# Kernel optimization log

Measured on AMD Instinct MI355X. Metric: run time of the kernel, lower is better.

## Reference

```python
import jax, jax.numpy as jnp
import numpy as np
from functools import partial

B, C, H, W = 16, 512, 38, 50
IMG_H, IMG_W = 608, 800
STRIDE = 16
IMG_SCALE = 1.0
MIN_SIZE = 16.0 * IMG_SCALE
PRE_NMS_TOP_N = 6000
POST_NMS_TOP_N = 300
NMS_THRESH = 0.7


def generate_anchor_base(base_size=16.0, ratios=(0.5, 1.0, 2.0), scales=(8.0, 16.0, 32.0)):
    # chainercv-style base anchors centered at (base/2, base/2), y1x1y2x2
    py = px = base_size / 2.0
    out = []
    for r in ratios:
        for s in scales:
            h = base_size * s * np.sqrt(r)
            w = base_size * s * np.sqrt(1.0 / r)
            out.append([py - h / 2, px - w / 2, py + h / 2, px + w / 2])
    return jnp.asarray(np.array(out, dtype=np.float32))  # [9, 4]


def all_anchors(anchor_base, stride, h, w):
    sy = jnp.arange(h, dtype=jnp.float32) * stride
    sx = jnp.arange(w, dtype=jnp.float32) * stride
    yy, xx = jnp.meshgrid(sy, sx, indexing='ij')
    shifts = jnp.stack([yy, xx, yy, xx], axis=-1).reshape(-1, 1, 4)  # [H*W,1,4]
    return (shifts + anchor_base[None]).reshape(-1, 4)  # [H*W*9, 4]


def conv2d(x, w, b, pad):
    y = jax.lax.conv_general_dilated(
        x, w, window_strides=(1, 1), padding=[(pad, pad), (pad, pad)],
        dimension_numbers=('NCHW', 'OIHW', 'NCHW'))
    return y + b[None, :, None, None]


def decode_boxes(anchors, loc):
    # anchors [N,4] y1x1y2x2, loc [B,N,4] (dy,dx,dh,dw)
    ah = anchors[:, 2] - anchors[:, 0]
    aw = anchors[:, 3] - anchors[:, 1]
    acy = anchors[:, 0] + 0.5 * ah
    acx = anchors[:, 1] + 0.5 * aw
    cy = loc[..., 0] * ah + acy
    cx = loc[..., 1] * aw + acx
    h = jnp.exp(loc[..., 2]) * ah
    w = jnp.exp(loc[..., 3]) * aw
    return jnp.stack([cy - 0.5 * h, cx - 0.5 * w, cy + 0.5 * h, cx + 0.5 * w], axis=-1)


def nms_fixed(boxes, scores, iou_thresh, max_out):
    # boxes [N,4], scores [N] (-inf = invalid); greedy NMS, fixed max_out steps
    areas = jnp.clip(boxes[:, 2] - boxes[:, 0], 0) * jnp.clip(boxes[:, 3] - boxes[:, 1], 0)

    def step(valid, _):
        s = jnp.where(valid, scores, -jnp.inf)
        i = jnp.argmax(s)
        ok = jnp.isfinite(s[i])
        box = boxes[i]
        yy1 = jnp.maximum(box[0], boxes[:, 0])
        xx1 = jnp.maximum(box[1], boxes[:, 1])
        yy2 = jnp.minimum(box[2], boxes[:, 2])
        xx2 = jnp.minimum(box[3], boxes[:, 3])
        inter = jnp.clip(yy2 - yy1, 0) * jnp.clip(xx2 - xx1, 0)
        iou = inter / (areas + areas[i] - inter + 1e-9)
        valid = valid & (iou <= iou_thresh)
        valid = valid.at[i].set(False)
        return valid, (i, ok)

    valid0 = jnp.isfinite(scores)
    _, (idx, ok) = jax.lax.scan(step, valid0, None, length=max_out)
    return idx, ok


def proposal_single(boxes, scores):
    # boxes [N,4], scores [N] for one image
    # clip to image
    boxes = jnp.stack([
        jnp.clip(boxes[:, 0], 0.0, IMG_H), jnp.clip(boxes[:, 1], 0.0, IMG_W),
        jnp.clip(boxes[:, 2], 0.0, IMG_H), jnp.clip(boxes[:, 3], 0.0, IMG_W)], axis=-1)
    hs = boxes[:, 2] - boxes[:, 0]
    ws = boxes[:, 3] - boxes[:, 1]
    keep = (hs >= MIN_SIZE) & (ws >= MIN_SIZE)
    scores = jnp.where(keep, scores, -jnp.inf)
    top_s, top_i = jax.lax.top_k(scores, PRE_NMS_TOP_N)
    top_b = boxes[top_i]
    idx, ok = nms_fixed(top_b, top_s, NMS_THRESH, POST_NMS_TOP_N)
    okf = ok.astype(boxes.dtype)
    rois = top_b[idx] * okf[:, None]
    rsc = jnp.where(ok, top_s[idx], 0.0)
    return jnp.concatenate([rois, rsc[:, None]], axis=-1)  # [POST, 5]


def setup_inputs() -> dict:
    key = jax.random.key(0)
    ks = jax.random.split(key, 7)
    return {
        'x': jax.random.normal(ks[0], (B, C, H, W), jnp.float32),
        'share_w': jax.random.normal(ks[1], (512, 512, 3, 3), jnp.float32) * 0.02,
        'share_b': jnp.zeros((512,), jnp.float32),
        'cls_w': jax.random.normal(ks[2], (18, 512, 1, 1), jnp.float32) * 0.02,
        'cls_b': jnp.zeros((18,), jnp.float32),
        'reg_w': jax.random.normal(ks[3], (36, 512, 1, 1), jnp.float32) * 0.02,
        'reg_b': jnp.zeros((36,), jnp.float32),
    }


def reference(x, share_w, share_b, cls_w, cls_b, reg_w, reg_b):
    anchors = all_anchors(generate_anchor_base(), STRIDE, H, W)  # [H*W*9, 4]
    shared = jax.nn.relu(conv2d(x, share_w, share_b, 1))
    cls = conv2d(shared, cls_w, cls_b, 0)           # [B,18,H,W]
    # note: original _reshape is a no-op (view result discarded), so softmax is over all 18 channels
    cls = jax.nn.softmax(cls, axis=1)
    reg = conv2d(shared, reg_w, reg_b, 0)           # [B,36,H,W]
    # foreground scores: [B,18,H,W] -> [B,H,W,9,2] -> fg channel
    scores = cls.transpose(0, 2, 3, 1).reshape(B, H * W * 9, 2)[..., 1]
    loc = reg.transpose(0, 2, 3, 1).reshape(B, H * W * 9, 4)
    boxes = decode_boxes(anchors, loc)              # [B,N,4]
    rois = jax.vmap(proposal_single)(boxes, scores)  # [B,POST,5]
    return rois
```

## Files before the change

kernel.cpp:

```cpp
#include <hip/hip_runtime.h>
#include <math.h>

#define NB 16
#define NC 512
#define NH 38
#define NW 50
#define NHW 1900
#define NPOS 30400
#define NANCH 17100
#define PRE_N 6000
#define POST_N 300
#define KTOT 4608
#define IMGH 608.0f
#define IMGW 800.0f

__global__ __launch_bounds__(256)
void conv_f64_v3(const float* __restrict__ x, const float* __restrict__ w,
                 const float* __restrict__ bias, float* __restrict__ out)
{
    const int b    = blockIdx.z;
    const int co0  = blockIdx.y * 128;
    const int pos0 = blockIdx.x * 64;

    __shared__ __align__(16) double Ad[8][130];
    __shared__ __align__(16) double Bd[8][66];

    const int tid = threadIdx.x;
    const int ty  = tid >> 4;
    const int tx  = tid & 15;

    double acc[8][4];
#pragma unroll
    for (int m = 0; m < 8; ++m)
#pragma unroll
        for (int n = 0; n < 4; ++n) acc[m][n] = 0.0;

    const float* xb = x + (size_t)b * NC * NHW;

    const int coiA = tid >> 1;
    const int k4A  = (tid & 1) * 4;
    const int kk2B = (tid >> 6) * 2;
    const int piB  = tid & 63;
    const int slotB = ((piB & 3) << 4) + (piB >> 2);
    const int pB   = pos0 + piB;
    const int pyB  = pB / NW;
    const int pxB  = pB - pyB * NW;

    for (int k0 = 0; k0 < KTOT; k0 += 8) {
        const float4 wa = *reinterpret_cast<const float4*>(
            &w[(size_t)(co0 + coiA) * KTOT + k0 + k4A]);
        float bs[2];
#pragma unroll
        for (int j = 0; j < 2; ++j) {
            const int k  = k0 + kk2B + j;
            const int ci = k / 9;
            const int rr = k - ci * 9;
            const int ky = rr / 3;
            const int kx = rr - ky * 3;
            const int yy = pyB + ky - 1;
            const int xx = pxB + kx - 1;
            float v = 0.f;
            if (pB < NHW && (unsigned)yy < (unsigned)NH && (unsigned)xx < (unsigned)NW)
                v = xb[(size_t)ci * NHW + yy * NW + xx];
            bs[j] = v;
        }
        __syncthreads();
        Ad[k4A + 0][coiA] = (double)wa.x;
        Ad[k4A + 1][coiA] = (double)wa.y;
        Ad[k4A + 2][coiA] = (double)wa.z;
        Ad[k4A + 3][coiA] = (double)wa.w;
        Bd[kk2B + 0][slotB] = (double)bs[0];
        Bd[kk2B + 1][slotB] = (double)bs[1];
        __syncthreads();

#pragma unroll
        for (int kk = 0; kk < 8; ++kk) {
            double av[8], bv[4];
#pragma unroll
            for (int m = 0; m < 8; ++m) av[m] = Ad[kk][ty * 8 + m];
#pragma unroll
            for (int n = 0; n < 4; ++n) bv[n] = Bd[kk][n * 16 + tx];
#pragma unroll
            for (int m = 0; m < 8; ++m)
#pragma unroll
                for (int n = 0; n < 4; ++n) acc[m][n] += av[m] * bv[n];
        }
        __syncthreads();
    }

    const int pos = pos0 + tx * 4;
#pragma unroll
    for (int m = 0; m < 8; ++m) {
        const int co = co0 + ty * 8 + m;
        const double bi = (double)bias[co];
        if (pos < NHW) {
            float* orow = out + ((size_t)b * NC + co) * NHW;
            float4 v;
            double d0 = acc[m][0] + bi;
            double d1 = acc[m][1] + bi;
            double d2 = acc[m][2] + bi;
            double d3 = acc[m][3] + bi;
            v.x = (float)(d0 > 0.0 ? d0 : 0.0);
            v.y = (float)(d1 > 0.0 ? d1 : 0.0);
            v.z = (float)(d2 > 0.0 ? d2 : 0.0);
            v.w = (float)(d3 > 0.0 ? d3 : 0.0);
            *reinterpret_cast<float4*>(&orow[pos]) = v;
        }
    }
}

__global__ __launch_bounds__(256)
void head_f64(const float* __restrict__ act,
              const float* __restrict__ cls_w, const float* __restrict__ cls_b,
              const float* __restrict__ reg_w, const float* __restrict__ reg_b,
              float* __restrict__ boxes, float* __restrict__ scores)
{
    const int p = blockIdx.x * 256 + threadIdx.x;
    if (p >= NPOS) return;
    const int b  = p / NHW;
    const int hw = p - b * NHW;

    const float* av = act + (size_t)b * NC * NHW + hw;

    double acc[54];
#pragma unroll
    for (int o = 0; o < 54; ++o) acc[o] = 0.0;

    for (int c = 0; c < NC; ++c) {
        const double v = (double)av[(size_t)c * NHW];
#pragma unroll
        for (int o = 0; o < 18; ++o) acc[o]      += v * (double)cls_w[o * NC + c];
#pragma unroll
        for (int o = 0; o < 36; ++o) acc[18 + o] += v * (double)reg_w[o * NC + c];
    }

    float lg[18];
#pragma unroll
    for (int o = 0; o < 18; ++o) lg[o] = (float)(acc[o] + (double)cls_b[o]);
    float loc[36];
#pragma unroll
    for (int o = 0; o < 36; ++o) loc[o] = (float)(acc[18 + o] + (double)reg_b[o]);

    double mx = -1e300;
#pragma unroll
    for (int o = 0; o < 18; ++o) mx = fmax(mx, (double)lg[o]);
    double sum = 0.0;
#pragma unroll
    for (int o = 0; o < 18; ++o) sum += exp((double)lg[o] - mx);
    const double inv = 1.0 / sum;

    const int hy = hw / NW;
    const int hx = hw - hy * NW;
    const float shy = (float)(hy * 16);
    const float shx = (float)(hx * 16);

    const double rats[3] = {0.5, 1.0, 2.0};
    const double scls[3] = {8.0, 16.0, 32.0};

#pragma unroll
    for (int a = 0; a < 9; ++a) {
        const int ir = a / 3, is = a - ir * 3;
        const double hh = 16.0 * scls[is] * sqrt(rats[ir]);
        const double wd = 16.0 * scls[is] * sqrt(1.0 / rats[ir]);
        const float ay1 = (float)(8.0 - hh * 0.5) + shy;
        const float ax1 = (float)(8.0 - wd * 0.5) + shx;
        const float ay2 = (float)(8.0 + hh * 0.5) + shy;
        const float ax2 = (float)(8.0 + wd * 0.5) + shx;
        const float ahf = ay2 - ay1;
        const float awf = ax2 - ax1;
        const float acy = ay1 + 0.5f * ahf;
        const float acx = ax1 + 0.5f * awf;

        const double ah = (double)ahf, aw = (double)awf;
        const double dy = (double)loc[4 * a + 0];
        const double dx = (double)loc[4 * a + 1];
        const double dh = (double)loc[4 * a + 2];
        const double dw = (double)loc[4 * a + 3];
        const double cy = dy * ah + (double)acy;
        const double cx = dx * aw + (double)acx;
        const double bh = exp(dh) * ah;
        const double bw = exp(dw) * aw;
        float y1 = (float)(cy - 0.5 * bh);
        float x1 = (float)(cx - 0.5 * bw);
        float y2 = (float)(cy + 0.5 * bh);
        float x2 = (float)(cx + 0.5 * bw);
        y1 = fminf(fmaxf(y1, 0.f), IMGH);
        y2 = fminf(fmaxf(y2, 0.f), IMGH);
        x1 = fminf(fmaxf(x1, 0.f), IMGW);
        x2 = fminf(fmaxf(x2, 0.f), IMGW);
        const bool keep = ((y2 - y1) >= 16.0f) && ((x2 - x1) >= 16.0f);

        float sc = (float)(exp((double)lg[2 * a + 1] - mx) * inv);
        if (!keep) sc = -INFINITY;

        const int n = hw * 9 + a;
        float4 bx; bx.x = y1; bx.y = x1; bx.z = y2; bx.w = x2;
        *reinterpret_cast<float4*>(&boxes[((size_t)b * NANCH + n) * 4]) = bx;
        scores[(size_t)b * NANCH + n] = sc;
    }
}

__global__ __launch_bounds__(256)
void rank2(const float* __restrict__ scores, const float* __restrict__ boxes,
           float* __restrict__ sortedS, float* __restrict__ sortedB)
{
    const int b = blockIdx.y;
    const int i = blockIdx.x * 256 + threadIdx.x;
    if (i >= NANCH) return;
    const float si = scores[(size_t)b * NANCH + i];
    const float* sb = scores + (size_t)b * NANCH;
    int rank = 0;
    for (int j = 0; j < NANCH; ++j) {
        const float sj = sb[j];
        rank += (sj > si) || (sj == si && j < i);
    }
    if (rank < PRE_N) {
        sortedS[(size_t)b * PRE_N + rank] = si;
        const float4 bx = *reinterpret_cast<const float4*>(&boxes[((size_t)b * NANCH + i) * 4]);
        *reinterpret_cast<float4*>(&sortedB[((size_t)b * PRE_N + rank) * 4]) = bx;
    }
}

__global__ __launch_bounds__(64)
void nms3(const float* __restrict__ sortedS, const float* __restrict__ sortedB,
          float* __restrict__ out)
{
    const int b    = blockIdx.x;
    const int lane = threadIdx.x;

    __shared__ float ky1[POST_N], kx1[POST_N], ky2[POST_N], kx2[POST_N];
    __shared__ float kar[POST_N], ksc[POST_N];
    __shared__ float cs[256];
    __shared__ float cb[256][4];

    const float* SS = sortedS + (size_t)b * PRE_N;
    const float* BB = sortedB + (size_t)b * PRE_N * 4;

    int nk = 0;
    bool done = false;
    for (int c0 = 0; c0 < PRE_N && !done; c0 += 256) {
        __syncthreads();
        for (int i = lane; i < 256; i += 64) {
            const int gi = c0 + i;
            if (gi < PRE_N) {
                cs[i] = SS[gi];
                const float4 bx = *reinterpret_cast<const float4*>(&BB[(size_t)gi * 4]);
                cb[i][0] = bx.x; cb[i][1] = bx.y; cb[i][2] = bx.z; cb[i][3] = bx.w;
            } else {
                cs[i] = -INFINITY;
                cb[i][0] = 0.f; cb[i][1] = 0.f; cb[i][2] = 0.f; cb[i][3] = 0.f;
            }
        }
        __syncthreads();

        for (int ic = 0; ic < 256; ++ic) {
            const float sc = cs[ic];
            if (sc == -INFINITY) { done = true; break; }
            const float y1 = cb[ic][0], x1 = cb[ic][1];
            const float y2 = cb[ic][2], x2 = cb[ic][3];
            const float areaC = fmaxf(y2 - y1, 0.f) * fmaxf(x2 - x1, 0.f);
            bool sup = false;
            for (int t = lane; t < nk; t += 64) {
                const float yy1 = fmaxf(y1, ky1[t]);
                const float xx1 = fmaxf(x1, kx1[t]);
                const float yy2 = fminf(y2, ky2[t]);
                const float xx2 = fminf(x2, kx2[t]);
                const float inter = fmaxf(yy2 - yy1, 0.f) * fmaxf(xx2 - xx1, 0.f);
                const float iou = inter / (areaC + kar[t] - inter + 1e-9f);
                if (iou > 0.7f) sup = true;
            }
            if (__ballot(sup) == 0ull) {
                if (lane == 0) {
                    ky1[nk] = y1; kx1[nk] = x1; ky2[nk] = y2; kx2[nk] = x2;
                    kar[nk] = areaC; ksc[nk] = sc;
                }
                __syncthreads();
                ++nk;
                if (nk == POST_N) { done = true; break; }
            }
        }
    }

    __syncthreads();
    for (int k2 = lane; k2 < POST_N; k2 += 64) {
        float o0 = 0.f, o1 = 0.f, o2 = 0.f, o3 = 0.f, o4 = 0.f;
        if (k2 < nk) {
            o0 = ky1[k2]; o1 = kx1[k2]; o2 = ky2[k2]; o3 = kx2[k2]; o4 = ksc[k2];
        }
        float* orow = out + ((size_t)b * POST_N + k2) * 5;
        orow[0] = o0; orow[1] = o1; orow[2] = o2; orow[3] = o3; orow[4] = o4;
    }
}

static const float* pick_input(void* const* d_in, const int* in_sizes, int n_in,
                               int want, int fallback)
{
    for (int i = 0; i < n_in; ++i)
        if (in_sizes[i] == want) return (const float*)d_in[i];
    return (const float*)d_in[fallback];
}

extern "C" void kernel_launch(void* const* d_in, const int* in_sizes, int n_in,
                              void* d_out, int out_size, void* d_ws, size_t ws_size,
                              hipStream_t stream)
{
    const float* x       = pick_input(d_in, in_sizes, n_in, 15564800, 0);
    const float* share_w = pick_input(d_in, in_sizes, n_in, 2359296, 1);
    const float* share_b = pick_input(d_in, in_sizes, n_in, 512, 2);
    const float* cls_w   = pick_input(d_in, in_sizes, n_in, 9216, 3);
    const float* cls_b   = pick_input(d_in, in_sizes, n_in, 18, 4);
    const float* reg_w   = pick_input(d_in, in_sizes, n_in, 18432, 5);
    const float* reg_b   = pick_input(d_in, in_sizes, n_in, 36, 6);
    float* out = (float*)d_out;

    float* W = (float*)d_ws;
    float* act     = W;
    float* boxes   = W + 15564800;
    float* scores  = W + 16659200;
    float* sortedB = W + 16932800;
    float* sortedS = W + 17316800;

    conv_f64_v3<<<dim3(30, 4, NB), 256, 0, stream>>>(x, share_w, share_b, act);

    head_f64<<<dim3(119), 256, 0, stream>>>(act, cls_w, cls_b, reg_w, reg_b,
                                            boxes, scores);

    rank2<<<dim3(67, 16), 256, 0, stream>>>(scores, boxes, sortedS, sortedB);

    nms3<<<dim3(16), 64, 0, stream>>>(sortedS, sortedB, out);
}
```

Measured before the change: 5.577 ms.

## Double-buffer conv shared tiles and replace per-k div/mod with incremental indices

The 3x3 conv GEMM kernel now double-buffers its A and B shared-memory tiles. Global loads for the next k-slice are issued before the FMA loop on the current slice, which cuts the barriers per iteration from two to one. The im2col index math changes from per-element division by 9 and 3 to incrementally stepped ci/ky/kx counters. Each thread now loads two pixels for one k row instead of one pixel for two k rows. This doubles shared memory use and adds register pressure, which may lower occupancy.

```diff
diff --git a/kernel.cpp b/kernel.cpp
--- a/kernel.cpp
+++ b/kernel.cpp
@@ -11,19 +11,20 @@
 #define PRE_N 6000
 #define POST_N 300
 #define KTOT 4608
+#define NIT 576
 #define IMGH 608.0f
 #define IMGW 800.0f
 
 __global__ __launch_bounds__(256)
-void conv_f64_v3(const float* __restrict__ x, const float* __restrict__ w,
+void conv_f64_v4(const float* __restrict__ x, const float* __restrict__ w,
                  const float* __restrict__ bias, float* __restrict__ out)
 {
     const int b    = blockIdx.z;
     const int co0  = blockIdx.y * 128;
     const int pos0 = blockIdx.x * 64;
 
-    __shared__ __align__(16) double Ad[8][130];
-    __shared__ __align__(16) double Bd[8][66];
+    __shared__ __align__(16) double Ad[2][8][130];
+    __shared__ __align__(16) double Bd[2][8][66];
 
     const int tid = threadIdx.x;
     const int ty  = tid >> 4;
@@ -39,53 +40,96 @@
 
     const int coiA = tid >> 1;
     const int k4A  = (tid & 1) * 4;
-    const int kk2B = (tid >> 6) * 2;
-    const int piB  = tid & 63;
-    const int slotB = ((piB & 3) << 4) + (piB >> 2);
-    const int pB   = pos0 + piB;
-    const int pyB  = pB / NW;
-    const int pxB  = pB - pyB * NW;
-
-    for (int k0 = 0; k0 < KTOT; k0 += 8) {
-        const float4 wa = *reinterpret_cast<const float4*>(
-            &w[(size_t)(co0 + coiA) * KTOT + k0 + k4A]);
-        float bs[2];
-#pragma unroll
-        for (int j = 0; j < 2; ++j) {
-            const int k  = k0 + kk2B + j;
-            const int ci = k / 9;
-            const int rr = k - ci * 9;
-            const int ky = rr / 3;
-            const int kx = rr - ky * 3;
-            const int yy = pyB + ky - 1;
-            const int xx = pxB + kx - 1;
-            float v = 0.f;
-            if (pB < NHW && (unsigned)yy < (unsigned)NH && (unsigned)xx < (unsigned)NW)
-                v = xb[(size_t)ci * NHW + yy * NW + xx];
-            bs[j] = v;
-        }
-        __syncthreads();
-        Ad[k4A + 0][coiA] = (double)wa.x;
-        Ad[k4A + 1][coiA] = (double)wa.y;
-        Ad[k4A + 2][coiA] = (double)wa.z;
-        Ad[k4A + 3][coiA] = (double)wa.w;
-        Bd[kk2B + 0][slotB] = (double)bs[0];
-        Bd[kk2B + 1][slotB] = (double)bs[1];
-        __syncthreads();
+    const float* wptr = w + (size_t)(co0 + coiA) * KTOT + k4A;
+
+    const int kkB   = tid >> 5;
+    const int piB   = tid & 31;
+    const int slot1 = ((piB & 3) << 4) + (piB >> 2);
+    const int slot2 = slot1 + 8;
+    const int pB1   = pos0 + piB;
+    const int pB2   = pos0 + piB + 32;
+    const int py1   = pB1 / NW, px1 = pB1 - (pB1 / NW) * NW;
+    const int py2   = pB2 / NW, px2 = pB2 - (pB2 / NW) * NW;
+    const bool ok1  = pB1 < NHW;
+    const bool ok2  = pB2 < NHW;
+
+    int ci = 0;
+    int ky = kkB / 3;
+    int kx = kkB - 3 * (kkB / 3);
+    const float* xci = xb;
+
+    float4 wa = *reinterpret_cast<const float4*>(wptr);
+    float bs0, bs1;
+    {
+        const int yy1 = py1 + ky - 1, xx1 = px1 + kx - 1;
+        const int yy2 = py2 + ky - 1, xx2 = px2 + kx - 1;
+        bs0 = (ok1 && (unsigned)yy1 < (unsigned)NH && (unsigned)xx1 < (unsigned)NW)
+                  ? xci[yy1 * NW + xx1] : 0.f;
+        bs1 = (ok2 && (unsigned)yy2 < (unsigned)NH && (unsigned)xx2 < (unsigned)NW)
+                  ? xci[yy2 * NW + xx2] : 0.f;
+    }
+    {
+        const bool wrap = (ky == 0) && (kx == 0);
+        if (wrap) { ky = 2; kx = 2; }
+        else {
+            --kx;
+            if (kx < 0) { kx = 2; --ky; }
+            ++ci; xci += NHW;
+        }
+    }
+    Ad[0][k4A + 0][coiA] = (double)wa.x;
+    Ad[0][k4A + 1][coiA] = (double)wa.y;
+    Ad[0][k4A + 2][coiA] = (double)wa.z;
+    Ad[0][k4A + 3][coiA] = (double)wa.w;
+    Bd[0][kkB][slot1] = (double)bs0;
+    Bd[0][kkB][slot2] = (double)bs1;
+    __syncthreads();
+
+    int cur = 0;
+    for (int it = 0; it < NIT; ++it) {
+        const bool more = (it + 1) < NIT;
+        if (more) {
+            wptr += 8;
+            wa = *reinterpret_cast<const float4*>(wptr);
+            const int yy1 = py1 + ky - 1, xx1 = px1 + kx - 1;
+            const int yy2 = py2 + ky - 1, xx2 = px2 + kx - 1;
+            bs0 = (ok1 && (unsigned)yy1 < (unsigned)NH && (unsigned)xx1 < (unsigned)NW)
+                      ? xci[yy1 * NW + xx1] : 0.f;
+            bs1 = (ok2 && (unsigned)yy2 < (unsigned)NH && (unsigned)xx2 < (unsigned)NW)
+                      ? xci[yy2 * NW + xx2] : 0.f;
+            const bool wrap = (ky == 0) && (kx == 0);
+            if (wrap) { ky = 2; kx = 2; }
+            else {
+                --kx;
+                if (kx < 0) { kx = 2; --ky; }
+                ++ci; xci += NHW;
+            }
+        }
 
 #pragma unroll
         for (int kk = 0; kk < 8; ++kk) {
             double av[8], bv[4];
 #pragma unroll
-            for (int m = 0; m < 8; ++m) av[m] = Ad[kk][ty * 8 + m];
-#pragma unroll
-            for (int n = 0; n < 4; ++n) bv[n] = Bd[kk][n * 16 + tx];
+            for (int m = 0; m < 8; ++m) av[m] = Ad[cur][kk][ty * 8 + m];
+#pragma unroll
+            for (int n = 0; n < 4; ++n) bv[n] = Bd[cur][kk][n * 16 + tx];
 #pragma unroll
             for (int m = 0; m < 8; ++m)
 #pragma unroll
                 for (int n = 0; n < 4; ++n) acc[m][n] += av[m] * bv[n];
         }
-        __syncthreads();
+
+        if (more) {
+            const int nb = cur ^ 1;
+            Ad[nb][k4A + 0][coiA] = (double)wa.x;
+            Ad[nb][k4A + 1][coiA] = (double)wa.y;
+            Ad[nb][k4A + 2][coiA] = (double)wa.z;
+            Ad[nb][k4A + 3][coiA] = (double)wa.w;
+            Bd[nb][kkB][slot1] = (double)bs0;
+            Bd[nb][kkB][slot2] = (double)bs1;
+            __syncthreads();
+        }
+        cur ^= 1;
     }
 
     const int pos = pos0 + tx * 4;
@@ -320,7 +364,7 @@
     float* sortedB = W + 16932800;
     float* sortedS = W + 17316800;
 
-    conv_f64_v3<<<dim3(30, 4, NB), 256, 0, stream>>>(x, share_w, share_b, act);
+    conv_f64_v4<<<dim3(30, 4, NB), 256, 0, stream>>>(x, share_w, share_b, act);
 
     head_f64<<<dim3(119), 256, 0, stream>>>(act, cls_w, cls_b, reg_w, reg_b,
                                             boxes, scores);
```

Result: no change. 5.499 ms (-1.4%).

## Give each wave private double-buffered LDS tiles and drop block barriers in conv

Applied to the files above, without the earlier changes.

The fp64 3x3 conv kernel is restructured so each of the four waves stages its own 32-channel A tile and its own copy of the 64-position B tile into private, double-buffered shared memory. This removes every __syncthreads from the main K loop. The im2col divisions by 9 and 3 are replaced by incrementally advanced (ky, kx, channel) state, and each lane now loads 8 input values per step. In exchange, input loads and B staging are repeated four times per block and LDS use grows, which may raise cache and LDS traffic or cut occupancy.

```diff
diff --git a/kernel.cpp b/kernel.cpp
--- a/kernel.cpp
+++ b/kernel.cpp
@@ -11,23 +11,26 @@
 #define PRE_N 6000
 #define POST_N 300
 #define KTOT 4608
+#define NIT 576
 #define IMGH 608.0f
 #define IMGW 800.0f
 
 __global__ __launch_bounds__(256)
-void conv_f64_v3(const float* __restrict__ x, const float* __restrict__ w,
+void conv_f64_v5(const float* __restrict__ x, const float* __restrict__ w,
                  const float* __restrict__ bias, float* __restrict__ out)
 {
     const int b    = blockIdx.z;
     const int co0  = blockIdx.y * 128;
     const int pos0 = blockIdx.x * 64;
 
-    __shared__ __align__(16) double Ad[8][130];
-    __shared__ __align__(16) double Bd[8][66];
-
-    const int tid = threadIdx.x;
-    const int ty  = tid >> 4;
-    const int tx  = tid & 15;
+    __shared__ __align__(16) double Ad[4][2][8][34];
+    __shared__ __align__(16) double Bd[4][2][8][66];
+
+    const int tid  = threadIdx.x;
+    const int wv   = tid >> 6;
+    const int lane = tid & 63;
+    const int tyw  = lane >> 4;
+    const int tx   = lane & 15;
 
     double acc[8][4];
 #pragma unroll
@@ -37,61 +40,100 @@
 
     const float* xb = x + (size_t)b * NC * NHW;
 
-    const int coiA = tid >> 1;
-    const int k4A  = (tid & 1) * 4;
-    const int kk2B = (tid >> 6) * 2;
-    const int piB  = tid & 63;
-    const int slotB = ((piB & 3) << 4) + (piB >> 2);
-    const int pB   = pos0 + piB;
-    const int pyB  = pB / NW;
-    const int pxB  = pB - pyB * NW;
-
-    for (int k0 = 0; k0 < KTOT; k0 += 8) {
-        const float4 wa = *reinterpret_cast<const float4*>(
-            &w[(size_t)(co0 + coiA) * KTOT + k0 + k4A]);
-        float bs[2];
-#pragma unroll
-        for (int j = 0; j < 2; ++j) {
-            const int k  = k0 + kk2B + j;
-            const int ci = k / 9;
-            const int rr = k - ci * 9;
-            const int ky = rr / 3;
-            const int kx = rr - ky * 3;
-            const int yy = pyB + ky - 1;
-            const int xx = pxB + kx - 1;
-            float v = 0.f;
-            if (pB < NHW && (unsigned)yy < (unsigned)NH && (unsigned)xx < (unsigned)NW)
-                v = xb[(size_t)ci * NHW + yy * NW + xx];
-            bs[j] = v;
-        }
-        __syncthreads();
-        Ad[k4A + 0][coiA] = (double)wa.x;
-        Ad[k4A + 1][coiA] = (double)wa.y;
-        Ad[k4A + 2][coiA] = (double)wa.z;
-        Ad[k4A + 3][coiA] = (double)wa.w;
-        Bd[kk2B + 0][slotB] = (double)bs[0];
-        Bd[kk2B + 1][slotB] = (double)bs[1];
-        __syncthreads();
+    const int coiA = lane >> 1;
+    const int k4A  = (lane & 1) * 4;
+    const float* wptr = w + (size_t)(co0 + wv * 32 + coiA) * KTOT + k4A;
+
+    const int slotB = ((lane & 3) << 4) + (lane >> 2);
+    const int pB    = pos0 + lane;
+    const bool okp  = pB < NHW;
+    const int pyB   = pB / NW;
+    const int pxB   = pB - pyB * NW;
+
+    int ky0 = 0, kx0 = 0;
+    const float* xci0 = xb;
+
+    float4 wa;
+    float  bs[8];
+
+#define LOAD_B()                                                              \
+    {                                                                         \
+        int ky = ky0, kx = kx0;                                               \
+        const float* xc = xci0;                                               \
+        _Pragma("unroll")                                                     \
+        for (int j = 0; j < 8; ++j) {                                         \
+            const int yy = pyB + ky - 1;                                      \
+            const int xx = pxB + kx - 1;                                      \
+            bs[j] = (okp && (unsigned)yy < (unsigned)NH &&                    \
+                     (unsigned)xx < (unsigned)NW) ? xc[yy * NW + xx] : 0.f;   \
+            ++kx;                                                             \
+            if (kx == 3) { kx = 0; ++ky; if (ky == 3) { ky = 0; xc += NHW; } }\
+        }                                                                     \
+    }
+
+#define ADV_STATE()                                                           \
+    {                                                                         \
+        const bool wrap = (ky0 == 0) && (kx0 == 0);                           \
+        if (wrap) { ky0 = 2; kx0 = 2; }                                       \
+        else {                                                                \
+            --kx0;                                                            \
+            if (kx0 < 0) { kx0 = 2; --ky0; }                                  \
+            xci0 += NHW;                                                      \
+        }                                                                     \
+    }
+
+#define STAGE(buf)                                                            \
+    {                                                                         \
+        Ad[wv][buf][k4A + 0][coiA] = (double)wa.x;                            \
+        Ad[wv][buf][k4A + 1][coiA] = (double)wa.y;                            \
+        Ad[wv][buf][k4A + 2][coiA] = (double)wa.z;                            \
+        Ad[wv][buf][k4A + 3][coiA] = (double)wa.w;                            \
+        _Pragma("unroll")                                                     \
+        for (int j = 0; j < 8; ++j) Bd[wv][buf][j][slotB] = (double)bs[j];    \
+    }
+
+    wa = *reinterpret_cast<const float4*>(wptr);
+    LOAD_B();
+    ADV_STATE();
+    STAGE(0);
+
+    int cur = 0;
+    for (int it = 0; it < NIT; ++it) {
+        const bool more = (it + 1) < NIT;
+        if (more) {
+            wptr += 8;
+            wa = *reinterpret_cast<const float4*>(wptr);
+            LOAD_B();
+            ADV_STATE();
+        }
 
 #pragma unroll
         for (int kk = 0; kk < 8; ++kk) {
             double av[8], bv[4];
 #pragma unroll
-            for (int m = 0; m < 8; ++m) av[m] = Ad[kk][ty * 8 + m];
-#pragma unroll
-            for (int n = 0; n < 4; ++n) bv[n] = Bd[kk][n * 16 + tx];
+            for (int m = 0; m < 8; ++m) av[m] = Ad[wv][cur][kk][tyw * 8 + m];
+#pragma unroll
+            for (int n = 0; n < 4; ++n) bv[n] = Bd[wv][cur][kk][n * 16 + tx];
 #pragma unroll
             for (int m = 0; m < 8; ++m)
 #pragma unroll
                 for (int n = 0; n < 4; ++n) acc[m][n] += av[m] * bv[n];
         }
-        __syncthreads();
-    }
+
+        if (more) {
+            const int nb = cur ^ 1;
+            STAGE(nb);
+        }
+        cur ^= 1;
+    }
+#undef LOAD_B
+#undef ADV_STATE
+#undef STAGE
 
     const int pos = pos0 + tx * 4;
 #pragma unroll
     for (int m = 0; m < 8; ++m) {
-        const int co = co0 + ty * 8 + m;
+        const int co = co0 + wv * 32 + tyw * 8 + m;
         const double bi = (double)bias[co];
         if (pos < NHW) {
             float* orow = out + ((size_t)b * NC + co) * NHW;
@@ -320,7 +362,7 @@
     float* sortedB = W + 16932800;
     float* sortedS = W + 17316800;
 
-    conv_f64_v3<<<dim3(30, 4, NB), 256, 0, stream>>>(x, share_w, share_b, act);
+    conv_f64_v5<<<dim3(30, 4, NB), 256, 0, stream>>>(x, share_w, share_b, act);
 
     head_f64<<<dim3(119), 256, 0, stream>>>(act, cls_w, cls_b, reg_w, reg_b,
                                             boxes, scores);
```

New measurement: 6.626 ms. 18.8% more time.
